# Kernel tuning notes

Hardware: AMD Instinct MI355X
Metric: run time of the kernel (lower is better)

The kernel has to match this reference:

```python
import jax, jax.numpy as jnp
import numpy as np

B, T, D, H = 2, 2048, 1024, 16
HD = D // H  # head dim = 64; rope half-dim = 32


def setup_inputs() -> dict:
    key = jax.random.key(0)
    ks = jax.random.split(key, 8)
    x = jax.random.normal(ks[0], (B, T, D), dtype=jnp.float32)
    # additive causal mask (upper triangle = -inf-like), as typically passed in
    mask = jnp.triu(jnp.full((T, T), -1e9, dtype=jnp.float32), k=1)
    # standard RoPE angles: theta = pos / 10000^(2i/hd)
    inv_freq = 1.0 / (10000.0 ** (np.arange(0, HD, 2, dtype=np.float32) / HD))
    ang = np.arange(T, dtype=np.float32)[:, None] * inv_freq[None, :]  # [T, HD//2]
    cos = jnp.asarray(np.cos(ang), dtype=jnp.float32)
    sin = jnp.asarray(np.sin(ang), dtype=jnp.float32)
    s = 1.0 / np.sqrt(D)
    Wq = jax.random.normal(ks[1], (D, D), dtype=jnp.float32) * s
    bq = jnp.zeros((D,), dtype=jnp.float32)
    Wk = jax.random.normal(ks[2], (D, D), dtype=jnp.float32) * s
    Wv = jax.random.normal(ks[3], (D, D), dtype=jnp.float32) * s
    bv = jnp.zeros((D,), dtype=jnp.float32)
    Wo = jax.random.normal(ks[4], (D, D), dtype=jnp.float32) * s
    bo = jnp.zeros((D,), dtype=jnp.float32)
    return {"x": x, "mask": mask, "cos": cos, "sin": sin, "Wq": Wq, "bq": bq,
            "Wk": Wk, "Wv": Wv, "bv": bv, "Wo": Wo, "bo": bo}


def _apply_rope(t, cos, sin):
    # t: [B, T, H, HD]; cos/sin: [T, HD//2]; complex multiply on (even, odd) pairs
    t = t.reshape(B, T, H, HD // 2, 2)
    t0, t1 = t[..., 0], t[..., 1]
    c = cos[None, :, None, :]
    s = sin[None, :, None, :]
    out = jnp.stack([t0 * c - t1 * s, t0 * s + t1 * c], axis=-1)
    return out.reshape(B, T, H, HD)


def reference(x, mask, cos, sin, Wq, bq, Wk, Wv, bv, Wo, bo):
    scale = float(HD) ** (-0.25)
    q = (x @ Wq.T + bq).reshape(B, T, H, HD)
    k = (x @ Wk.T).reshape(B, T, H, HD)  # key proj has no bias
    v = (x @ Wv.T + bv).reshape(B, T, H, HD)
    q = _apply_rope(q, cos, sin)
    k = _apply_rope(k, cos, sin)
    q = q.transpose(0, 2, 1, 3) * scale  # [B,H,T,HD]
    k = k.transpose(0, 2, 1, 3) * scale
    v = v.transpose(0, 2, 1, 3)
    qk = jnp.einsum("bhtd,bhsd->bhts", q, k) + mask  # [B,H,T,T]
    qk = qk.astype(jnp.float32)
    w = jax.nn.softmax(qk, axis=-1).astype(q.dtype)
    wv = jnp.einsum("bhts,bhsd->bhtd", w, v)
    wv = wv.transpose(0, 2, 1, 3).reshape(B, T, D)
    out = wv @ Wo.T + bo
    return out, qk
```

## Files before the change

### kernel.cpp

```cpp
#include <hip/hip_runtime.h>
#include <math.h>

#define Tc 2048
#define Dc 1024
#define Hc 16
#define HDc 64
#define BT 4096
#define SCALE 0.35355339059327379f

typedef _Float16 f16;
typedef __attribute__((ext_vector_type(4))) _Float16 f16x4;
typedef __attribute__((ext_vector_type(8))) _Float16 f16x8;
typedef __attribute__((ext_vector_type(4))) float f32x4;

__global__ __launch_bounds__(256)
void cast1_kernel(const float* __restrict__ in, f16* __restrict__ out, int n4)
{
    int i = blockIdx.x * 256 + threadIdx.x;
    if (i < n4) {
        float4 v = ((const float4*)in)[i];
        f16x4 o = {(f16)v.x, (f16)v.y, (f16)v.z, (f16)v.w};
        ((f16x4*)out)[i] = o;
    }
}

__global__ __launch_bounds__(256)
void cast4_kernel(const float* __restrict__ s0, const float* __restrict__ s1,
                  const float* __restrict__ s2, const float* __restrict__ s3,
                  f16* __restrict__ d0, f16* __restrict__ d1,
                  f16* __restrict__ d2, f16* __restrict__ d3, int n4)
{
    const float* s; f16* d;
    switch (blockIdx.y) {
        case 0:  s = s0; d = d0; break;
        case 1:  s = s1; d = d1; break;
        case 2:  s = s2; d = d2; break;
        default: s = s3; d = d3; break;
    }
    int i = blockIdx.x * 256 + threadIdx.x;
    if (i < n4) {
        float4 v = ((const float4*)s)[i];
        f16x4 o = {(f16)v.x, (f16)v.y, (f16)v.z, (f16)v.w};
        ((f16x4*)d)[i] = o;
    }
}

__global__ __launch_bounds__(256)
void qkv_proj_kernel(const f16* __restrict__ xh,
                     const f16* __restrict__ Wqh, const f16* __restrict__ Wkh,
                     const f16* __restrict__ Wvh,
                     const float* __restrict__ bq, const float* __restrict__ bv,
                     f16* __restrict__ qh, f16* __restrict__ kh, f16* __restrict__ vh,
                     const float* __restrict__ cosp, const float* __restrict__ sinp)
{
    const int mode = blockIdx.z;
    const f16* W = (mode == 0) ? Wqh : (mode == 1 ? Wkh : Wvh);
    const float* bias = (mode == 0) ? bq : (mode == 2 ? bv : nullptr);
    f16* dst = (mode == 0) ? qh : (mode == 1 ? kh : vh);

    __shared__ f16 As[128][40];
    __shared__ f16 Ws[64][40];
    const int tid = threadIdx.x;
    const int w = tid >> 6, l = tid & 63;
    const int lr = l & 15, lq = l >> 4;
    const int m0 = blockIdx.y * 128, n0 = blockIdx.x * 64;

    f32x4 acc[2][4] = {};

    for (int k0 = 0; k0 < Dc; k0 += 32) {
        __syncthreads();
        {
            int r = tid >> 1, c = (tid & 1) * 16;
            *(f16x8*)&As[r][c]     = *(const f16x8*)&xh[(size_t)(m0 + r) * Dc + k0 + c];
            *(f16x8*)&As[r][c + 8] = *(const f16x8*)&xh[(size_t)(m0 + r) * Dc + k0 + c + 8];
            int rw = tid >> 2, cw = (tid & 3) * 8;
            *(f16x8*)&Ws[rw][cw] = *(const f16x8*)&W[(size_t)(n0 + rw) * Dc + k0 + cw];
        }
        __syncthreads();
        f16x8 af[2], bf[4];
        #pragma unroll
        for (int mi = 0; mi < 2; mi++) af[mi] = *(const f16x8*)&As[32 * w + 16 * mi + lr][lq * 8];
        #pragma unroll
        for (int ni = 0; ni < 4; ni++) bf[ni] = *(const f16x8*)&Ws[16 * ni + lr][lq * 8];
        #pragma unroll
        for (int mi = 0; mi < 2; mi++)
            #pragma unroll
            for (int ni = 0; ni < 4; ni++)
                acc[mi][ni] = __builtin_amdgcn_mfma_f32_16x16x32_f16(af[mi], bf[ni], acc[mi][ni], 0, 0, 0);
    }

    #pragma unroll
    for (int mi = 0; mi < 2; mi++) {
        #pragma unroll
        for (int ni = 0; ni < 4; ni++) {
            #pragma unroll
            for (int i = 0; i < 4; i++) {
                int gm = m0 + 32 * w + 16 * mi + lq * 4 + i;
                int gn = n0 + 16 * ni + lr;
                float v = acc[mi][ni][i];
                if (bias) v += bias[gn];
                int b = gm >> 11, t = gm & 2047;
                int h = gn >> 6, d = gn & 63;
                if (mode != 2) {
                    float pv = __shfl_xor(v, 1, 64);
                    int p = d >> 1;
                    float c = cosp[t * 32 + p], s = sinp[t * 32 + p];
                    v = (d & 1) ? (pv * s + v * c) : (v * c - pv * s);
                    v *= SCALE;
                }
                dst[((size_t)(b * Hc + h) * Tc + t) * HDc + d] = (f16)v;
            }
        }
    }
}

__global__ __launch_bounds__(256)
void out_proj_kernel(const f16* __restrict__ A, const f16* __restrict__ W,
                     const float* __restrict__ bias, float* __restrict__ out)
{
    __shared__ f16 As[128][40];
    __shared__ f16 Ws[64][40];
    const int tid = threadIdx.x;
    const int w = tid >> 6, l = tid & 63;
    const int lr = l & 15, lq = l >> 4;
    const int m0 = blockIdx.y * 128, n0 = blockIdx.x * 64;

    f32x4 acc[2][4] = {};

    for (int k0 = 0; k0 < Dc; k0 += 32) {
        __syncthreads();
        {
            int r = tid >> 1, c = (tid & 1) * 16;
            *(f16x8*)&As[r][c]     = *(const f16x8*)&A[(size_t)(m0 + r) * Dc + k0 + c];
            *(f16x8*)&As[r][c + 8] = *(const f16x8*)&A[(size_t)(m0 + r) * Dc + k0 + c + 8];
            int rw = tid >> 2, cw = (tid & 3) * 8;
            *(f16x8*)&Ws[rw][cw] = *(const f16x8*)&W[(size_t)(n0 + rw) * Dc + k0 + cw];
        }
        __syncthreads();
        f16x8 af[2], bf[4];
        #pragma unroll
        for (int mi = 0; mi < 2; mi++) af[mi] = *(const f16x8*)&As[32 * w + 16 * mi + lr][lq * 8];
        #pragma unroll
        for (int ni = 0; ni < 4; ni++) bf[ni] = *(const f16x8*)&Ws[16 * ni + lr][lq * 8];
        #pragma unroll
        for (int mi = 0; mi < 2; mi++)
            #pragma unroll
            for (int ni = 0; ni < 4; ni++)
                acc[mi][ni] = __builtin_amdgcn_mfma_f32_16x16x32_f16(af[mi], bf[ni], acc[mi][ni], 0, 0, 0);
    }

    #pragma unroll
    for (int mi = 0; mi < 2; mi++)
        #pragma unroll
        for (int ni = 0; ni < 4; ni++)
            #pragma unroll
            for (int i = 0; i < 4; i++) {
                int gm = m0 + 32 * w + 16 * mi + lq * 4 + i;
                int gn = n0 + 16 * ni + lr;
                out[(size_t)gm * Dc + gn] = acc[mi][ni][i] + bias[gn];
            }
}

__global__ __launch_bounds__(256)
void flash_kernel(const f16* __restrict__ qh, const f16* __restrict__ kh,
                  const f16* __restrict__ vh, f16* __restrict__ wvh,
                  float* __restrict__ qk)
{
    const int z = blockIdx.y;
    const int t0 = (gridDim.x - 1 - blockIdx.x) * 64;
    const int tid = threadIdx.x;
    const int w = tid >> 6, l = tid & 63;
    const int lr = l & 15, lq = l >> 4;

    __shared__ f16 Qs[64][72];
    __shared__ f16 Ks[64][72];
    __shared__ f16 VsT[64][72];
    __shared__ f16 Ps[64][72];

    const f16* Qg = qh + (size_t)z * Tc * HDc;
    const f16* Kg = kh + (size_t)z * Tc * HDc;
    const f16* Vg = vh + (size_t)z * Tc * HDc;
    float* C = qk + (size_t)z * Tc * Tc;

    {
        int r = tid >> 2, c = (tid & 3) * 16;
        *(f16x8*)&Qs[r][c]     = *(const f16x8*)&Qg[(size_t)(t0 + r) * HDc + c];
        *(f16x8*)&Qs[r][c + 8] = *(const f16x8*)&Qg[(size_t)(t0 + r) * HDc + c + 8];
    }

    {
        int r = t0 + (tid >> 2);
        int n4 = (Tc - t0 - 64) >> 2;
        float4 mv; mv.x = mv.y = mv.z = mv.w = -1e9f;
        float4* rowp = (float4*)(C + (size_t)r * Tc + t0 + 64);
        for (int c = (tid & 3); c < n4; c += 4) rowp[c] = mv;
    }

    f32x4 O[4] = {};
    float mrow[4], lrow[4];
    #pragma unroll
    for (int i = 0; i < 4; i++) { mrow[i] = -1e30f; lrow[i] = 0.f; }

    for (int s0 = 0; s0 <= t0; s0 += 64) {
        __syncthreads();
        {
            int r = tid >> 2, c = (tid & 3) * 16;
            *(f16x8*)&Ks[r][c]     = *(const f16x8*)&Kg[(size_t)(s0 + r) * HDc + c];
            *(f16x8*)&Ks[r][c + 8] = *(const f16x8*)&Kg[(size_t)(s0 + r) * HDc + c + 8];
        }
        {
            int s = tid & 63, d0 = (tid >> 6) * 16;
            const f16* vp = &Vg[(size_t)(s0 + s) * HDc + d0];
            f16x8 v0 = *(const f16x8*)vp;
            f16x8 v1 = *(const f16x8*)(vp + 8);
            #pragma unroll
            for (int j = 0; j < 8; j++) {
                VsT[d0 + j][s]     = v0[j];
                VsT[d0 + 8 + j][s] = v1[j];
            }
        }
        __syncthreads();

        f32x4 S[4] = {};
        #pragma unroll
        for (int ks = 0; ks < 2; ks++) {
            f16x8 aq = *(const f16x8*)&Qs[16 * w + lr][lq * 8 + 32 * ks];
            #pragma unroll
            for (int ni = 0; ni < 4; ni++) {
                f16x8 bk = *(const f16x8*)&Ks[16 * ni + lr][lq * 8 + 32 * ks];
                S[ni] = __builtin_amdgcn_mfma_f32_16x16x32_f16(aq, bk, S[ni], 0, 0, 0);
            }
        }

        if (s0 == t0) {
            #pragma unroll
            for (int ni = 0; ni < 4; ni++)
                #pragma unroll
                for (int i = 0; i < 4; i++) {
                    int tg = t0 + 16 * w + lq * 4 + i;
                    int sg = s0 + 16 * ni + lr;
                    if (sg > tg) S[ni][i] = -1e9f;
                }
        }

        #pragma unroll
        for (int ni = 0; ni < 4; ni++)
            #pragma unroll
            for (int i = 0; i < 4; i++) {
                int tg = t0 + 16 * w + lq * 4 + i;
                int sg = s0 + 16 * ni + lr;
                C[(size_t)tg * Tc + sg] = S[ni][i];
            }

        #pragma unroll
        for (int i = 0; i < 4; i++) {
            float v = fmaxf(fmaxf(S[0][i], S[1][i]), fmaxf(S[2][i], S[3][i]));
            v = fmaxf(v, __shfl_xor(v, 1, 64));
            v = fmaxf(v, __shfl_xor(v, 2, 64));
            v = fmaxf(v, __shfl_xor(v, 4, 64));
            v = fmaxf(v, __shfl_xor(v, 8, 64));
            float mnew = fmaxf(mrow[i], v);
            float alpha = __expf(mrow[i] - mnew);
            mrow[i] = mnew;
            float rs = 0.f;
            #pragma unroll
            for (int ni = 0; ni < 4; ni++) {
                float p = __expf(S[ni][i] - mnew);
                S[ni][i] = p;
                rs += p;
            }
            rs += __shfl_xor(rs, 1, 64);
            rs += __shfl_xor(rs, 2, 64);
            rs += __shfl_xor(rs, 4, 64);
            rs += __shfl_xor(rs, 8, 64);
            lrow[i] = lrow[i] * alpha + rs;
            #pragma unroll
            for (int ni = 0; ni < 4; ni++) O[ni][i] *= alpha;
        }

        #pragma unroll
        for (int ni = 0; ni < 4; ni++)
            #pragma unroll
            for (int i = 0; i < 4; i++)
                Ps[16 * w + lq * 4 + i][16 * ni + lr] = (f16)S[ni][i];

        #pragma unroll
        for (int ks = 0; ks < 2; ks++) {
            f16x8 ap = *(const f16x8*)&Ps[16 * w + lr][lq * 8 + 32 * ks];
            #pragma unroll
            for (int ni = 0; ni < 4; ni++) {
                f16x8 bv = *(const f16x8*)&VsT[16 * ni + lr][lq * 8 + 32 * ks];
                O[ni] = __builtin_amdgcn_mfma_f32_16x16x32_f16(ap, bv, O[ni], 0, 0, 0);
            }
        }
    }

    const int b = z >> 4, h = z & 15;
    #pragma unroll
    for (int ni = 0; ni < 4; ni++)
        #pragma unroll
        for (int i = 0; i < 4; i++) {
            int tg = t0 + 16 * w + lq * 4 + i;
            int d = 16 * ni + lr;
            float o = O[ni][i] / lrow[i];
            wvh[((size_t)(b * Tc + tg)) * Dc + h * HDc + d] = (f16)o;
        }
}

extern "C" void kernel_launch(void* const* d_in, const int* in_sizes, int n_in,
                              void* d_out, int out_size, void* d_ws, size_t ws_size,
                              hipStream_t stream)
{
    const float* x    = (const float*)d_in[0];
    const float* cosp = (const float*)d_in[2];
    const float* sinp = (const float*)d_in[3];
    const float* Wq   = (const float*)d_in[4];
    const float* bq   = (const float*)d_in[5];
    const float* Wk   = (const float*)d_in[6];
    const float* Wv   = (const float*)d_in[7];
    const float* bv   = (const float*)d_in[8];
    const float* Wo   = (const float*)d_in[9];
    const float* bo   = (const float*)d_in[10];

    float* out = (float*)d_out;
    float* qk  = out + (size_t)BT * Dc;

    f16* ws  = (f16*)d_ws;
    f16* xh  = ws;
    f16* Wqh = xh  + (size_t)BT * Dc;
    f16* Wkh = Wqh + (size_t)Dc * Dc;
    f16* Wvh = Wkh + (size_t)Dc * Dc;
    f16* Woh = Wvh + (size_t)Dc * Dc;
    f16* qh  = Woh + (size_t)Dc * Dc;
    f16* kh  = qh  + (size_t)BT * Dc;
    f16* vh  = kh  + (size_t)BT * Dc;
    f16* wvh = vh  + (size_t)BT * Dc;

    dim3 blk(256);

    cast1_kernel<<<dim3(BT * Dc / 1024), blk, 0, stream>>>(x, xh, BT * Dc / 4);
    cast4_kernel<<<dim3(Dc * Dc / 1024, 4), blk, 0, stream>>>(
        Wq, Wk, Wv, Wo, Wqh, Wkh, Wvh, Woh, Dc * Dc / 4);

    qkv_proj_kernel<<<dim3(Dc / 64, BT / 128, 3), blk, 0, stream>>>(
        xh, Wqh, Wkh, Wvh, bq, bv, qh, kh, vh, cosp, sinp);

    flash_kernel<<<dim3(Tc / 64, 32), blk, 0, stream>>>(qh, kh, vh, wvh, qk);

    out_proj_kernel<<<dim3(Dc / 64, BT / 128), blk, 0, stream>>>(wvh, Woh, bo, out);
}
```

Baseline: 779.5 us.

## Rework GEMMs with 128x128 tiles, direct-to-LDS loads, and prefetch K/V in flash

The two cast kernels become one launch. The projection GEMMs switch to 128x128 block tiles with a 64-wide K step. Their tiles are loaded straight into LDS with global_load_lds into an XOR-swizzled layout, replacing the padded register-staged copies. The flash kernel now register-prefetches the next K/V tile while the current one is written to LDS, using raw barriers, which removes global load latency from the critical path. The flash kernel dominates runtime through its large qk write, so the gains are limited by that, and the raw-barrier ordering needs care.

```diff
diff --git a/kernel.cpp b/kernel.cpp
--- a/kernel.cpp
+++ b/kernel.cpp
@@ -13,37 +13,82 @@
 typedef __attribute__((ext_vector_type(8))) _Float16 f16x8;
 typedef __attribute__((ext_vector_type(4))) float f32x4;
 
+__device__ __forceinline__ void gload16(const f16* g, f16* l)
+{
+    __builtin_amdgcn_global_load_lds(
+        (const __attribute__((address_space(1))) void*)g,
+        (__attribute__((address_space(3))) void*)l, 16, 0, 0);
+}
+
 __global__ __launch_bounds__(256)
-void cast1_kernel(const float* __restrict__ in, f16* __restrict__ out, int n4)
-{
+void cast_kernel(const float* __restrict__ x,
+                 const float* __restrict__ Wq, const float* __restrict__ Wk,
+                 const float* __restrict__ Wv, const float* __restrict__ Wo,
+                 f16* __restrict__ xh,
+                 f16* __restrict__ Wqh, f16* __restrict__ Wkh,
+                 f16* __restrict__ Wvh, f16* __restrict__ Woh)
+{
+    const int u = blockIdx.y;
+    const float* s; f16* d;
+    if (u < 4) { s = x + (size_t)u * (1u << 20); d = xh + (size_t)u * (1u << 20); }
+    else switch (u) {
+        case 4:  s = Wq; d = Wqh; break;
+        case 5:  s = Wk; d = Wkh; break;
+        case 6:  s = Wv; d = Wvh; break;
+        default: s = Wo; d = Woh; break;
+    }
     int i = blockIdx.x * 256 + threadIdx.x;
-    if (i < n4) {
-        float4 v = ((const float4*)in)[i];
-        f16x4 o = {(f16)v.x, (f16)v.y, (f16)v.z, (f16)v.w};
-        ((f16x4*)out)[i] = o;
-    }
-}
-
-__global__ __launch_bounds__(256)
-void cast4_kernel(const float* __restrict__ s0, const float* __restrict__ s1,
-                  const float* __restrict__ s2, const float* __restrict__ s3,
-                  f16* __restrict__ d0, f16* __restrict__ d1,
-                  f16* __restrict__ d2, f16* __restrict__ d3, int n4)
-{
-    const float* s; f16* d;
-    switch (blockIdx.y) {
-        case 0:  s = s0; d = d0; break;
-        case 1:  s = s1; d = d1; break;
-        case 2:  s = s2; d = d2; break;
-        default: s = s3; d = d3; break;
-    }
-    int i = blockIdx.x * 256 + threadIdx.x;
-    if (i < n4) {
-        float4 v = ((const float4*)s)[i];
-        f16x4 o = {(f16)v.x, (f16)v.y, (f16)v.z, (f16)v.w};
-        ((f16x4*)d)[i] = o;
-    }
-}
+    float4 v = ((const float4*)s)[i];
+    f16x4 o = {(f16)v.x, (f16)v.y, (f16)v.z, (f16)v.w};
+    ((f16x4*)d)[i] = o;
+}
+
+#define GEMM_BODY(Aptr, Bptr)                                                        \
+    __shared__ f16 As[128][64];                                                      \
+    __shared__ f16 Bs[128][64];                                                      \
+    const int tid = threadIdx.x;                                                     \
+    const int w = tid >> 6, l = tid & 63;                                            \
+    const int lr = l & 15, lq = l >> 4;                                              \
+    const int wr = w >> 1, wc = w & 1;                                               \
+    const int m0 = blockIdx.y * 128, n0 = blockIdx.x * 128;                          \
+    const int srow8 = l >> 3, sslot = l & 7;                                         \
+    f32x4 acc[4][4] = {};                                                            \
+    for (int k0 = 0; k0 < Dc; k0 += 64) {                                            \
+        __syncthreads();                                                             \
+        _Pragma("unroll")                                                            \
+        for (int c = 0; c < 4; c++) {                                                \
+            int chunk = w * 4 + c;                                                   \
+            int row = chunk * 8 + srow8;                                             \
+            int col = (sslot ^ (row & 7)) * 8;                                       \
+            gload16(&Aptr[(size_t)(m0 + row) * Dc + k0 + col],                       \
+                    (f16*)((char*)&As[0][0] + chunk * 1024));                        \
+            gload16(&Bptr[(size_t)(n0 + row) * Dc + k0 + col],                       \
+                    (f16*)((char*)&Bs[0][0] + chunk * 1024));                        \
+        }                                                                            \
+        __syncthreads();                                                             \
+        _Pragma("unroll")                                                            \
+        for (int kk = 0; kk < 2; kk++) {                                             \
+            f16x8 af[4], bf[4];                                                      \
+            _Pragma("unroll")                                                        \
+            for (int mi = 0; mi < 4; mi++) {                                         \
+                int row = 64 * wr + 16 * mi + lr;                                    \
+                int bo = (lq * 16 + kk * 64) ^ ((row & 7) << 4);                     \
+                af[mi] = *(const f16x8*)((const char*)&As[0][0] + row * 128 + bo);   \
+            }                                                                        \
+            _Pragma("unroll")                                                        \
+            for (int ni = 0; ni < 4; ni++) {                                         \
+                int row = 64 * wc + 16 * ni + lr;                                    \
+                int bo = (lq * 16 + kk * 64) ^ ((row & 7) << 4);                     \
+                bf[ni] = *(const f16x8*)((const char*)&Bs[0][0] + row * 128 + bo);   \
+            }                                                                        \
+            _Pragma("unroll")                                                        \
+            for (int mi = 0; mi < 4; mi++)                                           \
+                _Pragma("unroll")                                                    \
+                for (int ni = 0; ni < 4; ni++)                                       \
+                    acc[mi][ni] = __builtin_amdgcn_mfma_f32_16x16x32_f16(            \
+                        af[mi], bf[ni], acc[mi][ni], 0, 0, 0);                       \
+        }                                                                            \
+    }
 
 __global__ __launch_bounds__(256)
 void qkv_proj_kernel(const f16* __restrict__ xh,
@@ -58,45 +103,16 @@
     const float* bias = (mode == 0) ? bq : (mode == 2 ? bv : nullptr);
     f16* dst = (mode == 0) ? qh : (mode == 1 ? kh : vh);
 
-    __shared__ f16 As[128][40];
-    __shared__ f16 Ws[64][40];
-    const int tid = threadIdx.x;
-    const int w = tid >> 6, l = tid & 63;
-    const int lr = l & 15, lq = l >> 4;
-    const int m0 = blockIdx.y * 128, n0 = blockIdx.x * 64;
-
-    f32x4 acc[2][4] = {};
-
-    for (int k0 = 0; k0 < Dc; k0 += 32) {
-        __syncthreads();
-        {
-            int r = tid >> 1, c = (tid & 1) * 16;
-            *(f16x8*)&As[r][c]     = *(const f16x8*)&xh[(size_t)(m0 + r) * Dc + k0 + c];
-            *(f16x8*)&As[r][c + 8] = *(const f16x8*)&xh[(size_t)(m0 + r) * Dc + k0 + c + 8];
-            int rw = tid >> 2, cw = (tid & 3) * 8;
-            *(f16x8*)&Ws[rw][cw] = *(const f16x8*)&W[(size_t)(n0 + rw) * Dc + k0 + cw];
-        }
-        __syncthreads();
-        f16x8 af[2], bf[4];
-        #pragma unroll
-        for (int mi = 0; mi < 2; mi++) af[mi] = *(const f16x8*)&As[32 * w + 16 * mi + lr][lq * 8];
-        #pragma unroll
-        for (int ni = 0; ni < 4; ni++) bf[ni] = *(const f16x8*)&Ws[16 * ni + lr][lq * 8];
-        #pragma unroll
-        for (int mi = 0; mi < 2; mi++)
-            #pragma unroll
-            for (int ni = 0; ni < 4; ni++)
-                acc[mi][ni] = __builtin_amdgcn_mfma_f32_16x16x32_f16(af[mi], bf[ni], acc[mi][ni], 0, 0, 0);
-    }
+    GEMM_BODY(xh, W)
 
     #pragma unroll
-    for (int mi = 0; mi < 2; mi++) {
+    for (int mi = 0; mi < 4; mi++) {
         #pragma unroll
         for (int ni = 0; ni < 4; ni++) {
             #pragma unroll
             for (int i = 0; i < 4; i++) {
-                int gm = m0 + 32 * w + 16 * mi + lq * 4 + i;
-                int gn = n0 + 16 * ni + lr;
+                int gm = m0 + 64 * wr + 16 * mi + lq * 4 + i;
+                int gn = n0 + 64 * wc + 16 * ni + lr;
                 float v = acc[mi][ni][i];
                 if (bias) v += bias[gn];
                 int b = gm >> 11, t = gm & 2047;
@@ -118,45 +134,16 @@
 void out_proj_kernel(const f16* __restrict__ A, const f16* __restrict__ W,
                      const float* __restrict__ bias, float* __restrict__ out)
 {
-    __shared__ f16 As[128][40];
-    __shared__ f16 Ws[64][40];
-    const int tid = threadIdx.x;
-    const int w = tid >> 6, l = tid & 63;
-    const int lr = l & 15, lq = l >> 4;
-    const int m0 = blockIdx.y * 128, n0 = blockIdx.x * 64;
-
-    f32x4 acc[2][4] = {};
-
-    for (int k0 = 0; k0 < Dc; k0 += 32) {
-        __syncthreads();
-        {
-            int r = tid >> 1, c = (tid & 1) * 16;
-            *(f16x8*)&As[r][c]     = *(const f16x8*)&A[(size_t)(m0 + r) * Dc + k0 + c];
-            *(f16x8*)&As[r][c + 8] = *(const f16x8*)&A[(size_t)(m0 + r) * Dc + k0 + c + 8];
-            int rw = tid >> 2, cw = (tid & 3) * 8;
-            *(f16x8*)&Ws[rw][cw] = *(const f16x8*)&W[(size_t)(n0 + rw) * Dc + k0 + cw];
-        }
-        __syncthreads();
-        f16x8 af[2], bf[4];
-        #pragma unroll
-        for (int mi = 0; mi < 2; mi++) af[mi] = *(const f16x8*)&As[32 * w + 16 * mi + lr][lq * 8];
-        #pragma unroll
-        for (int ni = 0; ni < 4; ni++) bf[ni] = *(const f16x8*)&Ws[16 * ni + lr][lq * 8];
-        #pragma unroll
-        for (int mi = 0; mi < 2; mi++)
-            #pragma unroll
-            for (int ni = 0; ni < 4; ni++)
-                acc[mi][ni] = __builtin_amdgcn_mfma_f32_16x16x32_f16(af[mi], bf[ni], acc[mi][ni], 0, 0, 0);
-    }
+    GEMM_BODY(A, W)
 
     #pragma unroll
-    for (int mi = 0; mi < 2; mi++)
+    for (int mi = 0; mi < 4; mi++)
         #pragma unroll
         for (int ni = 0; ni < 4; ni++)
             #pragma unroll
             for (int i = 0; i < 4; i++) {
-                int gm = m0 + 32 * w + 16 * mi + lq * 4 + i;
-                int gn = n0 + 16 * ni + lr;
+                int gm = m0 + 64 * wr + 16 * mi + lq * 4 + i;
+                int gn = n0 + 64 * wc + 16 * ni + lr;
                 out[(size_t)gm * Dc + gn] = acc[mi][ni][i] + bias[gn];
             }
 }
@@ -196,30 +183,43 @@
         for (int c = (tid & 3); c < n4; c += 4) rowp[c] = mv;
     }
 
+    const int kr = tid >> 2, kc = (tid & 3) * 16;
+    const int vs = tid & 63, vd = (tid >> 6) * 16;
+    f16x8 rk0 = *(const f16x8*)&Kg[(size_t)kr * HDc + kc];
+    f16x8 rk1 = *(const f16x8*)&Kg[(size_t)kr * HDc + kc + 8];
+    f16x8 rv0 = *(const f16x8*)&Vg[(size_t)vs * HDc + vd];
+    f16x8 rv1 = *(const f16x8*)&Vg[(size_t)vs * HDc + vd + 8];
+
     f32x4 O[4] = {};
     float mrow[4], lrow[4];
     #pragma unroll
     for (int i = 0; i < 4; i++) { mrow[i] = -1e30f; lrow[i] = 0.f; }
 
     for (int s0 = 0; s0 <= t0; s0 += 64) {
-        __syncthreads();
-        {
-            int r = tid >> 2, c = (tid & 3) * 16;
-            *(f16x8*)&Ks[r][c]     = *(const f16x8*)&Kg[(size_t)(s0 + r) * HDc + c];
-            *(f16x8*)&Ks[r][c + 8] = *(const f16x8*)&Kg[(size_t)(s0 + r) * HDc + c + 8];
-        }
-        {
-            int s = tid & 63, d0 = (tid >> 6) * 16;
-            const f16* vp = &Vg[(size_t)(s0 + s) * HDc + d0];
-            f16x8 v0 = *(const f16x8*)vp;
-            f16x8 v1 = *(const f16x8*)(vp + 8);
-            #pragma unroll
-            for (int j = 0; j < 8; j++) {
-                VsT[d0 + j][s]     = v0[j];
-                VsT[d0 + 8 + j][s] = v1[j];
-            }
-        }
-        __syncthreads();
+        asm volatile("" ::: "memory");
+        __builtin_amdgcn_s_barrier();
+        asm volatile("" ::: "memory");
+
+        *(f16x8*)&Ks[kr][kc]     = rk0;
+        *(f16x8*)&Ks[kr][kc + 8] = rk1;
+        #pragma unroll
+        for (int j = 0; j < 8; j++) {
+            VsT[vd + j][vs]     = rv0[j];
+            VsT[vd + 8 + j][vs] = rv1[j];
+        }
+
+        if (s0 + 64 <= t0) {
+            const f16* kp = &Kg[(size_t)(s0 + 64 + kr) * HDc + kc];
+            const f16* vp = &Vg[(size_t)(s0 + 64 + vs) * HDc + vd];
+            rk0 = *(const f16x8*)kp;
+            rk1 = *(const f16x8*)(kp + 8);
+            rv0 = *(const f16x8*)vp;
+            rv1 = *(const f16x8*)(vp + 8);
+        }
+
+        asm volatile("s_waitcnt lgkmcnt(0)" ::: "memory");
+        __builtin_amdgcn_s_barrier();
+        asm volatile("" ::: "memory");
 
         f32x4 S[4] = {};
         #pragma unroll
@@ -338,14 +338,13 @@
 
     dim3 blk(256);
 
-    cast1_kernel<<<dim3(BT * Dc / 1024), blk, 0, stream>>>(x, xh, BT * Dc / 4);
-    cast4_kernel<<<dim3(Dc * Dc / 1024, 4), blk, 0, stream>>>(
-        Wq, Wk, Wv, Wo, Wqh, Wkh, Wvh, Woh, Dc * Dc / 4);
-
-    qkv_proj_kernel<<<dim3(Dc / 64, BT / 128, 3), blk, 0, stream>>>(
+    cast_kernel<<<dim3(1024, 8), blk, 0, stream>>>(
+        x, Wq, Wk, Wv, Wo, xh, Wqh, Wkh, Wvh, Woh);
+
+    qkv_proj_kernel<<<dim3(Dc / 128, BT / 128, 3), blk, 0, stream>>>(
         xh, Wqh, Wkh, Wvh, bq, bv, qh, kh, vh, cosp, sinp);
 
     flash_kernel<<<dim3(Tc / 64, 32), blk, 0, stream>>>(qh, kh, vh, wvh, qk);
 
-    out_proj_kernel<<<dim3(Dc / 64, BT / 128), blk, 0, stream>>>(wvh, Woh, bo, out);
-}
+    out_proj_kernel<<<dim3(Dc / 128, BT / 128), blk, 0, stream>>>(wvh, Woh, bo, out);
+}
```

Measured after the change: 771.9 us. Within noise of the previous version (-1.0%).
